# Performance work log

Hardware: AMD Instinct MI355X
Metric: run time of the kernel (lower is better)

Reference implementation:

```python
import jax, jax.numpy as jnp
import numpy as np

N = 4096          # num_nodes
B = 16            # num_graphs (equal-sized contiguous segments)
L = 2             # max degree -> (L+1)**2 = 9 spherical components
NUM_DEG = (L + 1) ** 2
F = 128           # input feature dim
FQK = 128         # query/key feature dim
FV = 128          # value feature dim
MAX_FREQ = 8.0
MAX_LEN = 10.0

# degree index of each spherical component: [0, 1,1,1, 2,2,2,2,2]
DEG_IDX = np.array([l for l in range(L + 1) for _ in range(2 * l + 1)], dtype=np.int32)
# Lebedev grid num=6: octahedron vertices, equal weights 1/6
GRID_U = np.array([[1, 0, 0], [-1, 0, 0], [0, 1, 0], [0, -1, 0], [0, 0, 1], [0, 0, -1]], dtype=np.float32)
GRID_W = np.full((6,), 1.0 / 6.0, dtype=np.float32)


def _edense(x, W, b, deg_idx):
    y = jnp.einsum('npmf,mfg->npmg', x, W[deg_idx])
    return y.at[:, :, 0, :].add(b)


def _erope(x, cos, sin):
    # x: (N, 1, M9, Fqk); cos/sin: (N, G, H) with H = Fqk // 2
    x1 = x[:, None, :, :, 0::2]  # (N,1,1,M9,H) -> broadcast over G
    x2 = x[:, None, :, :, 1::2]
    c = cos[:, :, None, None, :]
    s = sin[:, :, None, None, :]
    r1 = x1 * c - x2 * s
    r2 = x1 * s + x2 * c
    out = jnp.stack([r1, r2], axis=-1)  # interleave pairs back
    return out.reshape(out.shape[:-2] + (-1,))  # (N, G, 1, M9, Fqk)


def setup_inputs() -> dict:
    key = jax.random.key(0)
    ks = jax.random.split(key, 8)
    inputs = jax.random.normal(ks[0], (N, 1, NUM_DEG, F), jnp.float32)
    positions = jax.random.normal(ks[1], (N, 3), jnp.float32) * 3.0
    # contiguous equal-sized graph segments (jraph-style padding convention)
    batch_segments = jnp.repeat(jnp.arange(B), N // B)
    graph_mask = jnp.ones((B,), bool)
    s = 1.0 / np.sqrt(F)
    Wq = jax.random.normal(ks[2], (L + 1, F, FQK), jnp.float32) * s
    Wk = jax.random.normal(ks[3], (L + 1, F, FQK), jnp.float32) * s
    Wv = jax.random.normal(ks[4], (L + 1, F, FV), jnp.float32) * s
    bq = jnp.zeros((FQK,), jnp.float32)
    bk = jnp.zeros((FQK,), jnp.float32)
    bv = jnp.zeros((FV,), jnp.float32)
    return dict(inputs=inputs, positions=positions, batch_segments=batch_segments,
                graph_mask=graph_mask, Wq=Wq, bq=bq, Wk=Wk, bk=bk, Wv=Wv, bv=bv)


def reference(inputs, positions, batch_segments, graph_mask, Wq, bq, Wk, bk, Wv, bv):
    deg_idx = jnp.asarray(DEG_IDX)
    grid_u = jnp.asarray(GRID_U)
    grid_w = jnp.asarray(GRID_W)
    G = grid_u.shape[0]
    # frequencies per frequency_init_fn: linspace(0, max_freq, Fqk/2) / max_length
    theta = jnp.linspace(0.0, MAX_FREQ, FQK // 2, dtype=jnp.float32) / MAX_LEN  # (H,)

    q = _edense(inputs, Wq, bq, deg_idx)  # (N,1,M9,FQK)
    k = _edense(inputs, Wk, bk, deg_idx)
    v = _edense(inputs, Wv, bv, deg_idx)  # (N,1,M9,FV)

    # Euclidean RoPE phases: angle[n,g,h] = (pos_n . u_g) * theta_h
    phase = positions @ grid_u.T           # (N,G)
    ang = phase[:, :, None] * theta        # (N,G,H)
    cos, sin = jnp.cos(ang), jnp.sin(ang)

    Mdim = NUM_DEG * FQK
    Ddim = NUM_DEG * FV
    qr = _erope(q, cos, sin).reshape(N, G, Mdim)  # (N,G,M)
    kr = _erope(k, cos, sin).reshape(N, G, Mdim)
    vf = v.reshape(N, Ddim)

    # per-graph linear attention with Lebedev quadrature (contiguous equal segments)
    n = N // B
    qr_b = qr.reshape(B, n, G, Mdim)
    kr_b = kr.reshape(B, n, G, Mdim)
    v_b = vf.reshape(B, n, Ddim)
    kv = jnp.einsum('bngm,bnd->bgmd', kr_b, v_b)          # KV summaries
    kv = kv * grid_w[None, :, None, None]                 # quadrature weights
    out = jnp.einsum('bngm,bgmd->bnd', qr_b, kv)          # integrate over grid
    out = out.reshape(N, 1, NUM_DEG, FV)
    mask = graph_mask[batch_segments]                     # (N,)
    return jnp.where(mask[:, None, None, None], out, 0.0)
```

## Files before the change

### kernel.cpp

```cpp
#include <hip/hip_runtime.h>


typedef unsigned short u16;
typedef __attribute__((ext_vector_type(8))) short short8;
typedef __attribute__((ext_vector_type(4))) float f32x4;

static constexpr int N_NODES = 4096;
static constexpr int NBATCH  = 16;
static constexpr int NB      = 256;
static constexpr int NDEG    = 9;
static constexpr int MD      = NDEG * 128;
static constexpr int KTOT    = 6 * MD;
static constexpr size_t ASLICE = (size_t)NBATCH * NB * NB;

static constexpr size_t OFF_WT  = 0;
static constexpr size_t OFF_QR  = OFF_WT  + (size_t)9*16384*2;
static constexpr size_t OFF_KR  = OFF_QR  + (size_t)N_NODES*KTOT*2;
static constexpr size_t OFF_VT  = OFF_KR  + (size_t)N_NODES*KTOT*2;
static constexpr size_t OFF_AP  = OFF_VT  + (size_t)N_NODES*MD*2;
static constexpr size_t OFF_A2  = OFF_QR;

__device__ inline u16 f2bf(float x) {
    union { float f; unsigned u; } v; v.f = x;
    unsigned r = v.u + 0x7fffu + ((v.u >> 16) & 1u);
    return (u16)(r >> 16);
}
__device__ inline float bf2f(u16 h) {
    union { unsigned u; float f; } v; v.u = ((unsigned)h) << 16; return v.f;
}
__device__ inline unsigned pk2bf(float a, float b) {
#if __has_builtin(__builtin_amdgcn_cvt_pk_bf16_f32)
    typedef __attribute__((ext_vector_type(2))) __bf16 bf2_t;
    union { bf2_t v; unsigned u; } cv;
    cv.v = __builtin_amdgcn_cvt_pk_bf16_f32(a, b);
    return cv.u;
#else
    return (unsigned)f2bf(a) | ((unsigned)f2bf(b) << 16);
#endif
}

__global__ __launch_bounds__(256) void k_prep(const float* __restrict__ Wq,
                                              const float* __restrict__ Wk,
                                              const float* __restrict__ Wv,
                                              u16* __restrict__ wt) {
    int t = blockIdx.x, tid = threadIdx.x;
    int blk = t >> 2, tt = t & 3;
    int mat = blk / 3, l = blk % 3;
    const float* W = (mat == 0 ? Wq : (mat == 1 ? Wk : Wv)) + (size_t)l * 16384;
    int j0 = (tt >> 1) * 64, f0 = (tt & 1) * 64;
    __shared__ u16 tile[64 * 72];
    for (int e = tid; e < 1024; e += 256) {
        int r = e >> 4, c = e & 15;
        float4 wv = *(const float4*)(W + (size_t)(f0 + r) * 128 + j0 + c * 4);
        tile[(c * 4 + 0) * 72 + r] = f2bf(wv.x);
        tile[(c * 4 + 1) * 72 + r] = f2bf(wv.y);
        tile[(c * 4 + 2) * 72 + r] = f2bf(wv.z);
        tile[(c * 4 + 3) * 72 + r] = f2bf(wv.w);
    }
    __syncthreads();
    u16* dst = wt + (size_t)blk * 16384;
    for (int e = tid; e < 512; e += 256) {
        int j = e >> 3, c = e & 7;
        *(uint4*)(dst + (size_t)(j0 + j) * 128 + f0 + c * 8) = *(const uint4*)(tile + j * 72 + c * 8);
    }
}

__global__ __launch_bounds__(256) void k_qkv(const float* __restrict__ X,
                                             const u16* __restrict__ wt,
                                             const float* __restrict__ bq,
                                             const float* __restrict__ bk,
                                             const float* __restrict__ bv,
                                             const float* __restrict__ pos,
                                             u16* __restrict__ qr,
                                             u16* __restrict__ kr,
                                             u16* __restrict__ vt) {
    const int nt = blockIdx.x, m = blockIdx.y, mat = blockIdx.z;
    const int n0 = nt * 64;
    const int deg = (m == 0) ? 0 : (m < 4 ? 1 : 2);
    const int tid = threadIdx.x;

    __shared__ u16 smem[26112];
    __shared__ float posS[192];
    u16* Xs = smem;
    u16* Ws = smem + 64 * 136;

    if (tid < 192) posS[tid] = pos[(size_t)n0 * 3 + tid];

    for (int e = tid; e < 2048; e += 256) {
        int r = e >> 5, f4 = e & 31;
        float4 xv = *(const float4*)(X + (size_t)(n0 + r) * MD + m * 128 + f4 * 4);
        uint2 o = make_uint2(pk2bf(xv.x, xv.y), pk2bf(xv.z, xv.w));
        *(uint2*)(Xs + r * 136 + f4 * 4) = o;
    }
    {
        const uint4* wsrc = (const uint4*)(wt + (size_t)(mat * 3 + deg) * 16384);
        for (int e = tid; e < 2048; e += 256) {
            int j = e >> 4, f8 = e & 15;
            *(uint4*)(Ws + j * 136 + f8 * 8) = wsrc[j * 16 + f8];
        }
    }
    __syncthreads();

    const int w = tid >> 6, lane = tid & 63, quad = lane >> 4, lrow = lane & 15;
    f32x4 acc[8];
#pragma unroll
    for (int ct = 0; ct < 8; ct++) acc[ct] = (f32x4){0.f, 0.f, 0.f, 0.f};
#pragma unroll
    for (int ks = 0; ks < 4; ks++) {
        short8 a = *(const short8*)(Xs + (w * 16 + lrow) * 136 + ks * 32 + quad * 8);
#pragma unroll
        for (int ct = 0; ct < 8; ct++) {
            short8 bfr = *(const short8*)(Ws + (ct * 16 + lrow) * 136 + ks * 32 + quad * 8);
            acc[ct] = __builtin_amdgcn_mfma_f32_16x16x32_bf16(a, bfr, acc[ct], 0, 0, 0);
        }
    }

    const float* bias = (mat == 0) ? bq : ((mat == 1) ? bk : bv);
    float yv[8][4];
#pragma unroll
    for (int ct = 0; ct < 8; ct++) {
        float bj = (m == 0) ? bias[ct * 16 + lrow] : 0.0f;
#pragma unroll
        for (int r = 0; r < 4; r++) yv[ct][r] = acc[ct][r] + bj;
    }

    if (mat == 2) {
        u16* T = Ws;
        const int nlb = w * 16 + quad * 4;
        __syncthreads();
#pragma unroll
        for (int ct = 0; ct < 8; ct++) {
            int j = ct * 16 + lrow;
            *(unsigned*)(T + j * 66 + nlb)     = pk2bf(yv[ct][0], yv[ct][1]);
            *(unsigned*)(T + j * 66 + nlb + 2) = pk2bf(yv[ct][2], yv[ct][3]);
        }
        __syncthreads();
        for (int e = tid; e < 1024; e += 256) {
            int d = e >> 3, c = e & 7;
            *(uint4*)(vt + (size_t)(m * 128 + d) * N_NODES + n0 + c * 8) =
                *(const uint4*)(T + d * 66 + c * 8);
        }
        return;
    }

    float pv[8][4];
#pragma unroll
    for (int ct = 0; ct < 8; ct++)
#pragma unroll
        for (int r = 0; r < 4; r++) pv[ct][r] = __shfl_xor(yv[ct][r], 1);

    float pr[4][3];
#pragma unroll
    for (int r = 0; r < 4; r++) {
        int nl = w * 16 + quad * 4 + r;
#pragma unroll
        for (int gp = 0; gp < 3; gp++) pr[r][gp] = posS[nl * 3 + gp];
    }
    const float thq = (float)(lrow >> 1) * (8.0f / 630.0f);
    const float th8 = 8.0f * (8.0f / 630.0f);

    u16* O0 = Xs;
    u16* O1 = Ws;
    u16* dst = (mat == 0) ? qr : kr;
    const bool even = !(lrow & 1);

    for (int gp = 0; gp < 3; gp++) {
        __syncthreads();
#pragma unroll
        for (int ct = 0; ct < 8; ct++) {
            float th = thq + (float)ct * th8;
#pragma unroll
            for (int r = 0; r < 4; r++) {
                int nl = w * 16 + quad * 4 + r;
                float s, c;
                __sincosf(pr[r][gp] * th, &s, &c);
                float t1 = yv[ct][r] * c, t2 = pv[ct][r] * s;
                float r0, r1;
                if (even) { r0 = t1 - t2; r1 = t1 + t2; }
                else      { r0 = t1 + t2; r1 = t1 - t2; }
                O0[nl * 136 + ct * 16 + lrow] = f2bf(r0);
                O1[nl * 136 + ct * 16 + lrow] = f2bf(r1);
            }
        }
        __syncthreads();
        for (int e = tid; e < 1024; e += 256) {
            int nl = e >> 4, c = e & 15;
            size_t o0 = ((size_t)(gp * 2) * N_NODES + n0 + nl) * MD + m * 128 + c * 8;
            *(uint4*)(dst + o0)                      = *(const uint4*)(O0 + nl * 136 + c * 8);
            *(uint4*)(dst + o0 + (size_t)N_NODES*MD) = *(const uint4*)(O1 + nl * 136 + c * 8);
        }
    }
}

__global__ __launch_bounds__(256) void k_gemm1(const u16* __restrict__ qr,
                                               const u16* __restrict__ kr,
                                               u16* __restrict__ Apart) {
    int idx = blockIdx.x;
    int grp = idx >> 6;
    int sub = idx & 63;
    int c   = sub & 7;
    int j   = sub >> 3;
    int bg  = grp * 4 + (c & 3);
    int g   = bg >> 4, b = bg & 15;
    int tr  = (c >> 2) * 2 + (j & 1);
    int tc  = j >> 1;

    int qn0 = b * NB + tr * 64, kn0 = b * NB + tc * 64;
    const size_t gbase = (size_t)g * N_NODES;
    int tid = threadIdx.x;
    __shared__ u16 Qs[64 * 72];
    __shared__ u16 Ks[64 * 72];
    int w = tid >> 6, lane = tid & 63, quad = lane >> 4, lrow = lane & 15;

    f32x4 acc[4];
#pragma unroll
    for (int ct = 0; ct < 4; ct++) acc[ct] = (f32x4){0.f, 0.f, 0.f, 0.f};

    for (int kc = 0; kc < MD / 64; kc++) {
        int k0 = kc * 64;
#pragma unroll
        for (int e = tid; e < 512; e += 256) {
            int r = e >> 3, s = e & 7;
            *(uint4*)(Qs + r * 72 + s * 8) = *(const uint4*)(qr + (gbase + qn0 + r) * MD + k0 + s * 8);
            *(uint4*)(Ks + r * 72 + s * 8) = *(const uint4*)(kr + (gbase + kn0 + r) * MD + k0 + s * 8);
        }
        __syncthreads();
#pragma unroll
        for (int ks = 0; ks < 2; ks++) {
            short8 a = *(const short8*)(Qs + (w * 16 + lrow) * 72 + ks * 32 + quad * 8);
#pragma unroll
            for (int ct = 0; ct < 4; ct++) {
                short8 bfr = *(const short8*)(Ks + (ct * 16 + lrow) * 72 + ks * 32 + quad * 8);
                acc[ct] = __builtin_amdgcn_mfma_f32_16x16x32_bf16(a, bfr, acc[ct], 0, 0, 0);
            }
        }
        __syncthreads();
    }
    u16* dst = Apart + ((size_t)g * NBATCH + b) * (NB * NB);
#pragma unroll
    for (int ct = 0; ct < 4; ct++)
#pragma unroll
        for (int r = 0; r < 4; r++) {
            int rib = tr * 64 + w * 16 + quad * 4 + r;
            int cib = tc * 64 + ct * 16 + lrow;
            dst[(size_t)rib * NB + cib] = f2bf(acc[ct][r]);
        }
}

__global__ __launch_bounds__(256) void k_asum(const u16* __restrict__ Ap,
                                              u16* __restrict__ A2) {
    size_t t = (size_t)blockIdx.x * 256 + threadIdx.x;
    float sacc[8];
#pragma unroll
    for (int i = 0; i < 8; i++) sacc[i] = 0.f;
#pragma unroll
    for (int s = 0; s < 6; s++) {
        uint4 v = *(const uint4*)(Ap + (size_t)s * ASLICE + t * 8);
        const unsigned* uu = (const unsigned*)&v;
#pragma unroll
        for (int h = 0; h < 4; h++) {
            sacc[h * 2]     += bf2f((u16)(uu[h] & 0xffff));
            sacc[h * 2 + 1] += bf2f((u16)(uu[h] >> 16));
        }
    }
    const float sc6 = 1.0f / 6.0f;
    unsigned o32[4];
#pragma unroll
    for (int i = 0; i < 4; i++) o32[i] = pk2bf(sacc[i * 2] * sc6, sacc[i * 2 + 1] * sc6);
    *(uint4*)(A2 + t * 8) = *(const uint4*)o32;
}

__global__ __launch_bounds__(256) void k_gemm2(const u16* __restrict__ A2,
                                               const u16* __restrict__ vt,
                                               const int* __restrict__ gmask,
                                               float* __restrict__ out) {
    int idx = blockIdx.x;
    int c   = idx & 7;
    int u   = idx >> 3;
    int pr9 = u / 9;
    int dcb = u - pr9 * 9;
    int pair = pr9 * 8 + c;
    int rt  = pair >> 4, b = pair & 15;
    int d0 = dcb * 128;
    int tid = threadIdx.x;
    __shared__ u16 As[64 * 72];
    __shared__ u16 Vs[128 * 72];
    int w = tid >> 6, lane = tid & 63, quad = lane >> 4, lrow = lane & 15;

    f32x4 acc[8];
#pragma unroll
    for (int ct = 0; ct < 8; ct++) acc[ct] = (f32x4){0.f, 0.f, 0.f, 0.f};

    for (int kc = 0; kc < 4; kc++) {
        int k0 = kc * 64;
#pragma unroll
        for (int e = tid; e < 512; e += 256) {
            int r = e >> 3, c8 = e & 7;
            *(uint4*)(As + r * 72 + c8 * 8) =
                *(const uint4*)(A2 + (size_t)b * (NB * NB) + (size_t)(rt * 64 + r) * NB + k0 + c8 * 8);
        }
#pragma unroll
        for (int e = tid; e < 1024; e += 256) {
            int rr = e >> 3, sc2 = e & 7;
            *(uint4*)(Vs + rr * 72 + sc2 * 8) =
                *(const uint4*)(vt + (size_t)(d0 + rr) * N_NODES + b * NB + k0 + sc2 * 8);
        }
        __syncthreads();
#pragma unroll
        for (int ks = 0; ks < 2; ks++) {
            short8 a = *(const short8*)(As + (w * 16 + lrow) * 72 + ks * 32 + quad * 8);
#pragma unroll
            for (int ct = 0; ct < 8; ct++) {
                short8 bfr = *(const short8*)(Vs + (ct * 16 + lrow) * 72 + ks * 32 + quad * 8);
                acc[ct] = __builtin_amdgcn_mfma_f32_16x16x32_bf16(a, bfr, acc[ct], 0, 0, 0);
            }
        }
        __syncthreads();
    }
    int mv = gmask[b];
#pragma unroll
    for (int ct = 0; ct < 8; ct++)
#pragma unroll
        for (int r = 0; r < 4; r++) {
            int node = b * NB + rt * 64 + w * 16 + quad * 4 + r;
            int d = d0 + ct * 16 + lrow;
            out[(size_t)node * MD + d] = mv ? acc[ct][r] : 0.0f;
        }
}

extern "C" void kernel_launch(void* const* d_in, const int* in_sizes, int n_in,
                              void* d_out, int out_size, void* d_ws, size_t ws_size,
                              hipStream_t stream) {
    (void)in_sizes; (void)n_in; (void)out_size; (void)ws_size;

    const float* X    = (const float*)d_in[0];
    const float* pos  = (const float*)d_in[1];
    const int*   gmask= (const int*)  d_in[3];
    const float* Wq   = (const float*)d_in[4];
    const float* bq   = (const float*)d_in[5];
    const float* Wk   = (const float*)d_in[6];
    const float* bk   = (const float*)d_in[7];
    const float* Wv   = (const float*)d_in[8];
    const float* bv   = (const float*)d_in[9];
    float* out = (float*)d_out;

    char* ws = (char*)d_ws;
    u16*   wt   = (u16*)  (ws + OFF_WT);
    u16*   qrp  = (u16*)  (ws + OFF_QR);
    u16*   krp  = (u16*)  (ws + OFF_KR);
    u16*   vtp  = (u16*)  (ws + OFF_VT);
    u16*   App  = (u16*)  (ws + OFF_AP);
    u16*   a2p  = (u16*)  (ws + OFF_A2);

    k_prep <<<dim3(36),         dim3(256), 0, stream>>>(Wq, Wk, Wv, wt);
    k_qkv  <<<dim3(64, 9, 3),   dim3(256), 0, stream>>>(X, wt, bq, bk, bv, pos, qrp, krp, vtp);
    k_gemm1<<<dim3(1536),       dim3(256), 0, stream>>>(qrp, krp, App);
    k_asum <<<dim3(512),        dim3(256), 0, stream>>>(App, a2p);
    k_gemm2<<<dim3(576),        dim3(256), 0, stream>>>(a2p, vtp, gmask, out);
}
```

Baseline: 171.2 us.

## Enlarge gemm1 tiles, split K in halves, and use direct global-to-LDS loads

The Q·K^T partial-score kernel now computes 128x128 output tiles per block instead of 64x64, and splits the 1152-long reduction into two halves written to separate partial slices. k_asum correspondingly sums 12 slices instead of 6. Tiles are loaded with global_load_lds straight into an XOR-swizzled, unpadded LDS layout. Separately, k_qkv loads its weight tile in two 64-row halves so its LDS footprint shrinks, which may raise occupancy. The aim is more reuse per loaded tile and less register staging, at the cost of doubling partial-score traffic and adding an extra barrier in k_qkv.

```diff
diff --git a/kernel.cpp b/kernel.cpp
--- a/kernel.cpp
+++ b/kernel.cpp
@@ -36,6 +36,17 @@
     return cv.u;
 #else
     return (unsigned)f2bf(a) | ((unsigned)f2bf(b) << 16);
+#endif
+}
+
+__device__ __forceinline__ void gl2lds16(const u16* g, u16* l) {
+#if __has_builtin(__builtin_amdgcn_global_load_lds)
+    __builtin_amdgcn_global_load_lds(
+        (const __attribute__((address_space(1))) unsigned int*)g,
+        (__attribute__((address_space(3))) unsigned int*)l, 16, 0, 0);
+#else
+    int lane = threadIdx.x & 63;
+    *(uint4*)(l + lane * 8) = *(const uint4*)g;
 #endif
 }
 
@@ -79,7 +90,7 @@
     const int deg = (m == 0) ? 0 : (m < 4 ? 1 : 2);
     const int tid = threadIdx.x;
 
-    __shared__ u16 smem[26112];
+    __shared__ u16 smem[2 * 64 * 136];
     __shared__ float posS[192];
     u16* Xs = smem;
     u16* Ws = smem + 64 * 136;
@@ -92,12 +103,10 @@
         uint2 o = make_uint2(pk2bf(xv.x, xv.y), pk2bf(xv.z, xv.w));
         *(uint2*)(Xs + r * 136 + f4 * 4) = o;
     }
-    {
-        const uint4* wsrc = (const uint4*)(wt + (size_t)(mat * 3 + deg) * 16384);
-        for (int e = tid; e < 2048; e += 256) {
-            int j = e >> 4, f8 = e & 15;
-            *(uint4*)(Ws + j * 136 + f8 * 8) = wsrc[j * 16 + f8];
-        }
+    const uint4* wsrc = (const uint4*)(wt + (size_t)(mat * 3 + deg) * 16384);
+    for (int e = tid; e < 1024; e += 256) {
+        int j = e >> 4, f8 = e & 15;
+        *(uint4*)(Ws + j * 136 + f8 * 8) = wsrc[j * 16 + f8];
     }
     __syncthreads();
 
@@ -105,14 +114,25 @@
     f32x4 acc[8];
 #pragma unroll
     for (int ct = 0; ct < 8; ct++) acc[ct] = (f32x4){0.f, 0.f, 0.f, 0.f};
-#pragma unroll
-    for (int ks = 0; ks < 4; ks++) {
-        short8 a = *(const short8*)(Xs + (w * 16 + lrow) * 136 + ks * 32 + quad * 8);
-#pragma unroll
-        for (int ct = 0; ct < 8; ct++) {
-            short8 bfr = *(const short8*)(Ws + (ct * 16 + lrow) * 136 + ks * 32 + quad * 8);
-            acc[ct] = __builtin_amdgcn_mfma_f32_16x16x32_bf16(a, bfr, acc[ct], 0, 0, 0);
-        }
+
+    for (int h = 0; h < 2; h++) {
+        if (h) {
+            for (int e = tid; e < 1024; e += 256) {
+                int j = e >> 4, f8 = e & 15;
+                *(uint4*)(Ws + j * 136 + f8 * 8) = wsrc[(64 + j) * 16 + f8];
+            }
+            __syncthreads();
+        }
+#pragma unroll
+        for (int ks = 0; ks < 4; ks++) {
+            short8 a = *(const short8*)(Xs + (w * 16 + lrow) * 136 + ks * 32 + quad * 8);
+#pragma unroll
+            for (int c4 = 0; c4 < 4; c4++) {
+                short8 bfr = *(const short8*)(Ws + (c4 * 16 + lrow) * 136 + ks * 32 + quad * 8);
+                acc[h * 4 + c4] = __builtin_amdgcn_mfma_f32_16x16x32_bf16(a, bfr, acc[h * 4 + c4], 0, 0, 0);
+            }
+        }
+        if (!h) __syncthreads();
     }
 
     const float* bias = (mat == 0) ? bq : ((mat == 1) ? bk : bv);
@@ -196,55 +216,71 @@
                                                const u16* __restrict__ kr,
                                                u16* __restrict__ Apart) {
     int idx = blockIdx.x;
-    int grp = idx >> 6;
-    int sub = idx & 63;
-    int c   = sub & 7;
-    int j   = sub >> 3;
-    int bg  = grp * 4 + (c & 3);
+    int c   = idx & 7;
+    int u   = idx >> 3;
+    int t   = u & 3;
+    int combo = (u >> 2) * 8 + c;
+    int kh  = combo & 1;
+    int bg  = combo >> 1;
     int g   = bg >> 4, b = bg & 15;
-    int tr  = (c >> 2) * 2 + (j & 1);
-    int tc  = j >> 1;
-
-    int qn0 = b * NB + tr * 64, kn0 = b * NB + tc * 64;
+    int tr  = t >> 1, tc = t & 1;
+
+    int qn0 = b * NB + tr * 128, kn0 = b * NB + tc * 128;
     const size_t gbase = (size_t)g * N_NODES;
     int tid = threadIdx.x;
-    __shared__ u16 Qs[64 * 72];
-    __shared__ u16 Ks[64 * 72];
+    __shared__ u16 Qs[128 * 64];
+    __shared__ u16 Ks[128 * 64];
     int w = tid >> 6, lane = tid & 63, quad = lane >> 4, lrow = lane & 15;
-
-    f32x4 acc[4];
-#pragma unroll
-    for (int ct = 0; ct < 4; ct++) acc[ct] = (f32x4){0.f, 0.f, 0.f, 0.f};
-
-    for (int kc = 0; kc < MD / 64; kc++) {
-        int k0 = kc * 64;
-#pragma unroll
-        for (int e = tid; e < 512; e += 256) {
-            int r = e >> 3, s = e & 7;
-            *(uint4*)(Qs + r * 72 + s * 8) = *(const uint4*)(qr + (gbase + qn0 + r) * MD + k0 + s * 8);
-            *(uint4*)(Ks + r * 72 + s * 8) = *(const uint4*)(kr + (gbase + kn0 + r) * MD + k0 + s * 8);
+    int l8 = lane >> 3, c8 = (lane & 7) * 8, lhi = lane >> 5;
+
+    f32x4 acc[2][8];
+#pragma unroll
+    for (int at = 0; at < 2; at++)
+#pragma unroll
+        for (int ct = 0; ct < 8; ct++) acc[at][ct] = (f32x4){0.f, 0.f, 0.f, 0.f};
+
+    const u16* qbase = qr + (gbase + qn0) * MD;
+    const u16* kbase = kr + (gbase + kn0) * MD;
+    u16* qdst = Qs + w * 32 * 64;
+    u16* kdst = Ks + w * 32 * 64;
+    const int fs = ((lrow >> 2) & 3) << 4;
+
+    for (int kc = 0; kc < 9; kc++) {
+        int k0 = kh * 576 + kc * 64;
+#pragma unroll
+        for (int s = 0; s < 4; s++) {
+            int row = w * 32 + s * 8 + l8;
+            int sc  = c8 ^ (((2 * s + lhi) & 3) << 4);
+            gl2lds16(qbase + (size_t)row * MD + k0 + sc, qdst + s * 8 * 64);
+            gl2lds16(kbase + (size_t)row * MD + k0 + sc, kdst + s * 8 * 64);
         }
         __syncthreads();
 #pragma unroll
         for (int ks = 0; ks < 2; ks++) {
-            short8 a = *(const short8*)(Qs + (w * 16 + lrow) * 72 + ks * 32 + quad * 8);
-#pragma unroll
-            for (int ct = 0; ct < 4; ct++) {
-                short8 bfr = *(const short8*)(Ks + (ct * 16 + lrow) * 72 + ks * 32 + quad * 8);
-                acc[ct] = __builtin_amdgcn_mfma_f32_16x16x32_bf16(a, bfr, acc[ct], 0, 0, 0);
-            }
-        }
-        __syncthreads();
-    }
-    u16* dst = Apart + ((size_t)g * NBATCH + b) * (NB * NB);
-#pragma unroll
-    for (int ct = 0; ct < 4; ct++)
-#pragma unroll
-        for (int r = 0; r < 4; r++) {
-            int rib = tr * 64 + w * 16 + quad * 4 + r;
-            int cib = tc * 64 + ct * 16 + lrow;
-            dst[(size_t)rib * NB + cib] = f2bf(acc[ct][r]);
-        }
+            int cs = (ks * 32 + quad * 8) ^ fs;
+            int r0 = w * 32 + lrow;
+            short8 a0 = *(const short8*)(Qs + r0 * 64 + cs);
+            short8 a1 = *(const short8*)(Qs + (r0 + 16) * 64 + cs);
+#pragma unroll
+            for (int ct = 0; ct < 8; ct++) {
+                short8 bfr = *(const short8*)(Ks + (ct * 16 + lrow) * 64 + cs);
+                acc[0][ct] = __builtin_amdgcn_mfma_f32_16x16x32_bf16(a0, bfr, acc[0][ct], 0, 0, 0);
+                acc[1][ct] = __builtin_amdgcn_mfma_f32_16x16x32_bf16(a1, bfr, acc[1][ct], 0, 0, 0);
+            }
+        }
+        __syncthreads();
+    }
+    u16* dst = Apart + ((size_t)(g * 2 + kh) * NBATCH + b) * (NB * NB);
+#pragma unroll
+    for (int at = 0; at < 2; at++)
+#pragma unroll
+        for (int ct = 0; ct < 8; ct++)
+#pragma unroll
+            for (int r = 0; r < 4; r++) {
+                int rib = tr * 128 + w * 32 + at * 16 + quad * 4 + r;
+                int cib = tc * 128 + ct * 16 + lrow;
+                dst[(size_t)rib * NB + cib] = f2bf(acc[at][ct][r]);
+            }
 }
 
 __global__ __launch_bounds__(256) void k_asum(const u16* __restrict__ Ap,
@@ -254,7 +290,7 @@
 #pragma unroll
     for (int i = 0; i < 8; i++) sacc[i] = 0.f;
 #pragma unroll
-    for (int s = 0; s < 6; s++) {
+    for (int s = 0; s < 12; s++) {
         uint4 v = *(const uint4*)(Ap + (size_t)s * ASLICE + t * 8);
         const unsigned* uu = (const unsigned*)&v;
 #pragma unroll
@@ -354,7 +390,7 @@
 
     k_prep <<<dim3(36),         dim3(256), 0, stream>>>(Wq, Wk, Wv, wt);
     k_qkv  <<<dim3(64, 9, 3),   dim3(256), 0, stream>>>(X, wt, bq, bk, bv, pos, qrp, krp, vtp);
-    k_gemm1<<<dim3(1536),       dim3(256), 0, stream>>>(qrp, krp, App);
+    k_gemm1<<<dim3(768),        dim3(256), 0, stream>>>(qrp, krp, App);
     k_asum <<<dim3(512),        dim3(256), 0, stream>>>(App, a2p);
     k_gemm2<<<dim3(576),        dim3(256), 0, stream>>>(a2p, vtp, gmask, out);
 }
```

Result: faster. 163.4 us (-4.5%).
